# Optimization experiments

Hardware: AMD Instinct MI355X
Metric: run time of the kernel (lower is better)

Reference implementation:

```python
import jax, jax.numpy as jnp
import numpy as np

HIDDEN = 4096
N_HEADS = 32
N_KV = 8
HEAD_DIM = HIDDEN // N_HEADS  # 128
EPS = 1e-6
THETA = 10000.0
T = 2048


def _rms_norm(x, w, eps=EPS):
    # x: [T, H, D]; normalize over last dim
    var = jnp.mean(jnp.square(x), axis=-1, keepdims=True)
    return x * jax.lax.rsqrt(var + eps) * w


def _rope(pos, q, k, theta=THETA):
    # pos: [T] int; q: [T, Hq, D]; k: [T, Hk, D]  (rotate-half / NeoX style)
    d = q.shape[-1]
    inv_freq = 1.0 / (theta ** (jnp.arange(0, d, 2, dtype=jnp.float32) / d))  # [D/2]
    ang = pos.astype(jnp.float32)[:, None] * inv_freq  # [T, D/2]
    cos = jnp.cos(ang)[:, None, :]  # [T, 1, D/2]
    sin = jnp.sin(ang)[:, None, :]

    def rot(x):
        x1, x2 = jnp.split(x, 2, axis=-1)
        return jnp.concatenate([x1 * cos - x2 * sin, x2 * cos + x1 * sin], axis=-1)

    return rot(q), rot(k)


def setup_inputs() -> dict:
    key = jax.random.key(0)
    ks = jax.random.split(key, 4)
    x = jax.random.normal(ks[0], (T, HIDDEN), dtype=jnp.float32)
    pos = jnp.arange(T, dtype=jnp.int32)
    qkv_w = jax.random.normal(ks[1], (HIDDEN, HEAD_DIM * (N_HEADS + 2 * N_KV)), dtype=jnp.float32) * (HIDDEN ** -0.5)
    q_norm_w = jnp.ones((HEAD_DIM,), dtype=jnp.float32)
    k_norm_w = jnp.ones((HEAD_DIM,), dtype=jnp.float32)
    o_w = jax.random.normal(ks[2], (HIDDEN, HIDDEN), dtype=jnp.float32) * (HIDDEN ** -0.5)
    return {"x": x, "pos": pos, "qkv_w": qkv_w, "q_norm_w": q_norm_w,
            "k_norm_w": k_norm_w, "o_w": o_w}


def reference(x, pos, qkv_w, q_norm_w, k_norm_w, o_w):
    q_size = N_HEADS * HEAD_DIM
    kv_size = N_KV * HEAD_DIM
    qkv = x @ qkv_w  # [T, q+2kv]
    q, k, v = jnp.split(qkv, [q_size, q_size + kv_size], axis=-1)
    q = q.reshape(T, N_HEADS, HEAD_DIM)
    k = k.reshape(T, N_KV, HEAD_DIM)
    v = v.reshape(T, N_KV, HEAD_DIM)
    # per-head RMSNorm on q/k (qkv_bias=False path)
    q = _rms_norm(q, q_norm_w)
    k = _rms_norm(k, k_norm_w)
    q, k = _rope(pos, q, k)
    # GQA: expand kv heads to query heads
    g = N_HEADS // N_KV
    k = jnp.repeat(k, g, axis=1)  # [T, Hq, D]
    v = jnp.repeat(v, g, axis=1)
    scale = HEAD_DIM ** -0.5
    scores = jnp.einsum('thd,shd->hts', q, k) * scale  # [H, T, T]
    causal = jnp.tril(jnp.ones((T, T), dtype=bool))
    scores = jnp.where(causal[None], scores, jnp.finfo(scores.dtype).min)
    p = jax.nn.softmax(scores, axis=-1)
    o = jnp.einsum('hts,shd->thd', p, v).reshape(T, HIDDEN)
    return o @ o_w
```

## Files before the change

kernel.cpp:

```cpp
#include <hip/hip_runtime.h>
#include <hip/hip_bf16.h>

using u16 = unsigned short;
typedef __bf16 bf16x8 __attribute__((ext_vector_type(8)));
typedef float f32x4 __attribute__((ext_vector_type(4)));
typedef u16 u16x8 __attribute__((ext_vector_type(8)));
typedef u16 u16x4 __attribute__((ext_vector_type(4)));

constexpr int T_SEQ = 2048;
constexpr int HID   = 4096;
constexpr int NH    = 32;
constexpr int NKV   = 8;
constexpr int HD    = 128;
constexpr int QKVN  = 6144;

__device__ __forceinline__ u16 f2b(float x) {
  return __builtin_bit_cast(u16, __float2bfloat16(x));
}
__device__ __forceinline__ float b2f(u16 u) {
  return __builtin_bit_cast(float, (unsigned int)u << 16);
}
__device__ __forceinline__ bf16x8 load8(const u16* p) {
  return __builtin_bit_cast(bf16x8, *reinterpret_cast<const u16x8*>(p));
}
__device__ __forceinline__ f32x4 mfma16(bf16x8 a, bf16x8 b, f32x4 c) {
  return __builtin_amdgcn_mfma_f32_16x16x32_bf16(a, b, c, 0, 0, 0);
}

__global__ __launch_bounds__(256) void k_cast_bf16(const float* __restrict__ in,
                                                   u16* __restrict__ out, int n4) {
  int i = blockIdx.x * 256 + threadIdx.x;
  if (i < n4) {
    float4 v = reinterpret_cast<const float4*>(in)[i];
    u16x4 o;
    o.x = f2b(v.x); o.y = f2b(v.y); o.z = f2b(v.z); o.w = f2b(v.w);
    reinterpret_cast<u16x4*>(out)[i] = o;
  }
}

__global__ __launch_bounds__(256) void k_transpose_cast(const float* __restrict__ in,
                                                        u16* __restrict__ out,
                                                        int R, int C) {
  __shared__ float tile[32][33];
  int cc = blockIdx.x << 5, rr = blockIdx.y << 5;
  int lx = threadIdx.x & 31, ly = threadIdx.x >> 5;
#pragma unroll
  for (int i = 0; i < 32; i += 8)
    tile[ly + i][lx] = in[(size_t)(rr + ly + i) * C + cc + lx];
  __syncthreads();
#pragma unroll
  for (int i = 0; i < 32; i += 8)
    out[(size_t)(cc + ly + i) * R + rr + lx] = f2b(tile[lx][ly + i]);
}

template <int N, int K, typename OutT>
__global__ __launch_bounds__(256) void k_gemm_bt(const u16* __restrict__ A,
                                                 const u16* __restrict__ B,
                                                 OutT* __restrict__ C) {
  __shared__ u16 lA[128 * 32];
  __shared__ u16 lB[128 * 32];
  const int tid = threadIdx.x;
  const int wid = tid >> 6, lane = tid & 63;
  const int row0 = blockIdx.y << 7, col0 = blockIdx.x << 7;
  const int wr = wid >> 1, wc = wid & 1;
  const int g = lane >> 4, c = lane & 15;

  f32x4 acc[4][4] = {};

  const int r_st = lane >> 2;
  const int slot_st = lane & 3;

  const int rA0 = wr * 64 + c;
  const int rB0 = wc * 64 + c;
  const int swzA = (rA0 >> 1) & 3;
  const int swzB = (rB0 >> 1) & 3;

  for (int kt = 0; kt < K / 32; ++kt) {
    const int kk = kt * 32;
#pragma unroll
    for (int i = 0; i < 2; ++i) {
      int r = wid * 16 + i * 64 + r_st;
      int s = slot_st ^ ((r >> 1) & 3);
      const u16* ga = A + (size_t)(row0 + r) * K + kk + s * 8;
      const u16* gb = B + (size_t)(col0 + r) * K + kk + s * 8;
      char* la = (char*)lA + wid * 1024 + i * 4096;
      char* lb = (char*)lB + wid * 1024 + i * 4096;
      __builtin_amdgcn_global_load_lds((const __attribute__((address_space(1))) void*)ga,
                                       (__attribute__((address_space(3))) void*)la, 16, 0, 0);
      __builtin_amdgcn_global_load_lds((const __attribute__((address_space(1))) void*)gb,
                                       (__attribute__((address_space(3))) void*)lb, 16, 0, 0);
    }
    __syncthreads();

    bf16x8 af[4], bfr[4];
#pragma unroll
    for (int m = 0; m < 4; ++m) {
      int row = rA0 + m * 16;
      af[m] = load8(lA + row * 32 + (g ^ swzA) * 8);
    }
#pragma unroll
    for (int n = 0; n < 4; ++n) {
      int row = rB0 + n * 16;
      bfr[n] = load8(lB + row * 32 + (g ^ swzB) * 8);
    }
#pragma unroll
    for (int m = 0; m < 4; ++m)
#pragma unroll
      for (int n = 0; n < 4; ++n)
        acc[m][n] = mfma16(af[m], bfr[n], acc[m][n]);
    __syncthreads();
  }

#pragma unroll
  for (int m = 0; m < 4; ++m) {
    int grow0 = row0 + wr * 64 + m * 16 + g * 4;
#pragma unroll
    for (int n = 0; n < 4; ++n) {
      int gcol = col0 + wc * 64 + n * 16 + c;
#pragma unroll
      for (int j = 0; j < 4; ++j) {
        float v = acc[m][n][j];
        if constexpr (sizeof(OutT) == 2)
          C[(size_t)(grow0 + j) * N + gcol] = f2b(v);
        else
          C[(size_t)(grow0 + j) * N + gcol] = v;
      }
    }
  }
}

__global__ __launch_bounds__(256) void k_normrope(const u16* __restrict__ qkv,
                                                  const int* __restrict__ pos,
                                                  const float* __restrict__ qw,
                                                  const float* __restrict__ kw,
                                                  u16* __restrict__ qo,
                                                  u16* __restrict__ ko,
                                                  u16* __restrict__ vo) {
  int t = blockIdx.x;
  int wid = threadIdx.x >> 6, lane = threadIdx.x & 63;
  int h = blockIdx.y * 4 + wid;
  const u16* src = qkv + (size_t)t * QKVN + h * HD;
  float x1 = b2f(src[lane]), x2 = b2f(src[lane + 64]);
  float ss = x1 * x1 + x2 * x2;
#pragma unroll
  for (int m = 1; m < 64; m <<= 1) ss += __shfl_xor(ss, m);
  float sc = rsqrtf(ss * (1.0f / HD) + 1e-6f);
  if (h < 40) {
    const float* w = (h < NH) ? qw : kw;
    float y1 = x1 * sc * w[lane], y2 = x2 * sc * w[lane + 64];
    float p = (float)pos[t];
    float inv = exp2f((float)lane * (-13.287712379549449f / 64.0f));
    float ang = p * inv;
    float sn, cs;
    sincosf(ang, &sn, &cs);
    float o1 = y1 * cs - y2 * sn;
    float o2 = y2 * cs + y1 * sn;
    if (h < NH) {
      o1 *= 0.08838834764831845f;
      o2 *= 0.08838834764831845f;
      u16* dst = qo + ((size_t)t * NH + h) * HD;
      dst[lane] = f2b(o1);
      dst[lane + 64] = f2b(o2);
    } else {
      u16* dst = ko + ((size_t)t * NKV + (h - NH)) * HD;
      dst[lane] = f2b(o1);
      dst[lane + 64] = f2b(o2);
    }
  } else {
    u16* dst = vo + ((size_t)t * NKV + (h - 40)) * HD;
    dst[lane] = f2b(x1);
    dst[lane + 64] = f2b(x2);
  }
}

__global__ __launch_bounds__(256) void k_transpose_v(const u16* __restrict__ vb,
                                                     u16* __restrict__ vt) {
  __shared__ u16 tile[32][33];
  int tt = blockIdx.x << 5, dd = blockIdx.y << 5, h = blockIdx.z;
  int lx = threadIdx.x & 31, ly = threadIdx.x >> 5;
#pragma unroll
  for (int i = 0; i < 32; i += 8)
    tile[ly + i][lx] = vb[((size_t)(tt + ly + i) * NKV + h) * HD + dd + lx];
  __syncthreads();
#pragma unroll
  for (int i = 0; i < 32; i += 8)
    vt[((size_t)h * HD + dd + ly + i) * T_SEQ + tt + lx] = tile[lx][ly + i];
}

__global__ __launch_bounds__(256) void k_attn(const u16* __restrict__ qb,
                                              const u16* __restrict__ kbg,
                                              const u16* __restrict__ vtg,
                                              u16* __restrict__ out) {
  __shared__ u16 sK[2][64 * 128];
  __shared__ u16 sV[2][128 * 64];
  const int wid = threadIdx.x >> 6, lane = threadIdx.x & 63;
  const int h = blockIdx.y, hk = h >> 2;
  const int qt = gridDim.x - 1 - blockIdx.x;
  const int ntiles = qt + 1;
  const int qb0 = qt * 64 + wid * 16;
  const int g = lane >> 4, c = lane & 15;

  auto stage = [&](int buf, int kvb) {
#pragma unroll
    for (int ii = 0; ii < 4; ++ii) {
      int i = wid * 4 + ii;
      {
        int r = i * 4 + (lane >> 4);
        int slot = lane & 15;
        const u16* src = kbg + ((size_t)(kvb + r) * NKV + hk) * HD + ((slot ^ (r & 15)) * 8);
        __builtin_amdgcn_global_load_lds((const __attribute__((address_space(1))) void*)src,
                                         (__attribute__((address_space(3))) void*)((char*)sK[buf] + i * 1024),
                                         16, 0, 0);
      }
      {
        int d = i * 8 + (lane >> 3);
        int slot3 = lane & 7;
        const u16* src = vtg + ((size_t)hk * HD + d) * T_SEQ + kvb + ((slot3 ^ (d & 7)) * 8);
        __builtin_amdgcn_global_load_lds((const __attribute__((address_space(1))) void*)src,
                                         (__attribute__((address_space(3))) void*)((char*)sV[buf] + i * 1024),
                                         16, 0, 0);
      }
    }
  };

  bf16x8 qf[4];
  const u16* qrow = qb + ((size_t)(qb0 + c) * NH + h) * HD;
#pragma unroll
  for (int kc = 0; kc < 4; ++kc) qf[kc] = load8(qrow + kc * 32 + g * 8);

  f32x4 accO[8] = {};
  float m_ = -1e30f, l_ = 0.f;
  const int tq = qb0 + c;

  const int gh = g >> 1, gl4 = 4 * (g & 1), cx = c & 7;
  const int e0 = ((0 + gh) ^ cx) * 8 + gl4;
  const int e1 = ((2 + gh) ^ cx) * 8 + gl4;
  const int e2 = ((4 + gh) ^ cx) * 8 + gl4;
  const int e3 = ((6 + gh) ^ cx) * 8 + gl4;

  stage(0, 0);
  __syncthreads();

  for (int kt = 0; kt < ntiles; ++kt) {
    const int kvb = kt * 64;
    const int cur = kt & 1;
    if (kt + 1 < ntiles) stage(cur ^ 1, kvb + 64);

    f32x4 s[4];
#pragma unroll
    for (int tt = 0; tt < 4; ++tt) {
      const u16* kr = sK[cur] + (tt * 16 + c) * 128;
      f32x4 st = {0.f, 0.f, 0.f, 0.f};
#pragma unroll
      for (int kc = 0; kc < 4; ++kc) {
        int slot = (kc * 4 + g) ^ c;
        st = mfma16(load8(kr + slot * 8), qf[kc], st);
      }
      s[tt] = st;
    }

    float vmax = -1e30f;
#pragma unroll
    for (int tt = 0; tt < 4; ++tt)
#pragma unroll
      for (int j = 0; j < 4; ++j) {
        int tk = kvb + tt * 16 + 4 * g + j;
        float v = (tk <= tq) ? s[tt][j] : -1e30f;
        s[tt][j] = v;
        vmax = fmaxf(vmax, v);
      }
    vmax = fmaxf(vmax, __shfl_xor(vmax, 16));
    vmax = fmaxf(vmax, __shfl_xor(vmax, 32));
    float mn = fmaxf(m_, vmax);
    float a = __expf(m_ - mn);
    float ps = 0.f;
#pragma unroll
    for (int tt = 0; tt < 4; ++tt)
#pragma unroll
      for (int j = 0; j < 4; ++j) {
        float p = __expf(s[tt][j] - mn);
        s[tt][j] = p;
        ps += p;
      }
    ps += __shfl_xor(ps, 16);
    ps += __shfl_xor(ps, 32);
    l_ = l_ * a + ps;
    m_ = mn;

    float aq[4];
#pragma unroll
    for (int j = 0; j < 4; ++j) aq[j] = __shfl(a, 20 * g + j);
#pragma unroll
    for (int c2 = 0; c2 < 8; ++c2)
#pragma unroll
      for (int j = 0; j < 4; ++j) accO[c2][j] *= aq[j];

    u16x8 p0u, p1u;
#pragma unroll
    for (int j = 0; j < 4; ++j) {
      p0u[j]     = f2b(s[0][j]);
      p0u[j + 4] = f2b(s[1][j]);
      p1u[j]     = f2b(s[2][j]);
      p1u[j + 4] = f2b(s[3][j]);
    }
    bf16x8 p0 = __builtin_bit_cast(bf16x8, p0u);
    bf16x8 p1 = __builtin_bit_cast(bf16x8, p1u);

#pragma unroll
    for (int c2 = 0; c2 < 8; ++c2) {
      const u16* vr = sV[cur] + (c2 * 16 + c) * 64;
      u16x4 va  = *reinterpret_cast<const u16x4*>(vr + e0);
      u16x4 vb4 = *reinterpret_cast<const u16x4*>(vr + e1);
      u16x4 vc4 = *reinterpret_cast<const u16x4*>(vr + e2);
      u16x4 vd  = *reinterpret_cast<const u16x4*>(vr + e3);
      u16x8 v0u, v1u;
#pragma unroll
      for (int j = 0; j < 4; ++j) {
        v0u[j] = va[j];  v0u[j + 4] = vb4[j];
        v1u[j] = vc4[j]; v1u[j + 4] = vd[j];
      }
      accO[c2] = mfma16(p0, __builtin_bit_cast(bf16x8, v0u), accO[c2]);
      accO[c2] = mfma16(p1, __builtin_bit_cast(bf16x8, v1u), accO[c2]);
    }

    __syncthreads();
  }

  float lq[4];
#pragma unroll
  for (int j = 0; j < 4; ++j) lq[j] = 1.0f / __shfl(l_, 20 * g + j);
#pragma unroll
  for (int c2 = 0; c2 < 8; ++c2)
#pragma unroll
    for (int j = 0; j < 4; ++j) {
      float o = accO[c2][j] * lq[j];
      out[(size_t)(qb0 + 4 * g + j) * HID + h * HD + c2 * 16 + c] = f2b(o);
    }
}

extern "C" void kernel_launch(void* const* d_in, const int* in_sizes, int n_in,
                              void* d_out, int out_size, void* d_ws, size_t ws_size,
                              hipStream_t stream) {
  (void)in_sizes; (void)n_in; (void)out_size; (void)ws_size;
  const float* x      = (const float*)d_in[0];
  const int*   pos    = (const int*)d_in[1];
  const float* qkv_w  = (const float*)d_in[2];
  const float* qnw    = (const float*)d_in[3];
  const float* knw    = (const float*)d_in[4];
  const float* ow     = (const float*)d_in[5];
  float* out = (float*)d_out;
  char* ws = (char*)d_ws;

  u16* xb   = (u16*)(ws + 0);
  u16* attn = (u16*)(ws + 0);
  char* B0 = ws + 16777216;
  u16* qkv_wt = (u16*)B0;
  u16* qbuf = (u16*)(B0 + 0);
  u16* kbuf = (u16*)(B0 + 16777216);
  u16* vbuf = (u16*)(B0 + 20971520);
  u16* vtb  = (u16*)(B0 + 25165824);
  char* C0 = ws + 67108864;
  u16* qkvb = (u16*)C0;
  u16* o_wt = (u16*)C0;

  k_cast_bf16<<<dim3((T_SEQ * HID / 4 + 255) / 256), 256, 0, stream>>>(x, xb, T_SEQ * HID / 4);
  k_transpose_cast<<<dim3(QKVN / 32, HID / 32), 256, 0, stream>>>(qkv_w, qkv_wt, HID, QKVN);
  k_gemm_bt<QKVN, HID, u16><<<dim3(QKVN / 128, T_SEQ / 128), 256, 0, stream>>>(xb, qkv_wt, qkvb);
  k_normrope<<<dim3(T_SEQ, 12), 256, 0, stream>>>(qkvb, pos, qnw, knw, qbuf, kbuf, vbuf);
  k_transpose_v<<<dim3(T_SEQ / 32, HD / 32, NKV), 256, 0, stream>>>(vbuf, vtb);
  k_transpose_cast<<<dim3(HID / 32, HID / 32), 256, 0, stream>>>(ow, o_wt, HID, HID);
  k_attn<<<dim3(T_SEQ / 64, NH), 256, 0, stream>>>(qbuf, kbuf, vtb, attn);
  k_gemm_bt<HID, HID, float><<<dim3(HID / 128, T_SEQ / 128), 256, 0, stream>>>(attn, o_wt, out);
}
```

Measured before the change: 610.3 us.

## Replace GEMM with 256x256-tile 8-wave double-buffered pipelined kernel

```diff
diff --git a/kernel.cpp b/kernel.cpp
--- a/kernel.cpp
+++ b/kernel.cpp
@@ -26,6 +26,11 @@
 __device__ __forceinline__ f32x4 mfma16(bf16x8 a, bf16x8 b, f32x4 c) {
   return __builtin_amdgcn_mfma_f32_16x16x32_bf16(a, b, c, 0, 0, 0);
 }
+__device__ __forceinline__ void gload_lds16(const u16* src, u16* dst) {
+  __builtin_amdgcn_global_load_lds((const __attribute__((address_space(1))) void*)src,
+                                   (__attribute__((address_space(3))) void*)dst, 16, 0, 0);
+}
+#define BAR() asm volatile("s_barrier" ::: "memory")
 
 __global__ __launch_bounds__(256) void k_cast_bf16(const float* __restrict__ in,
                                                    u16* __restrict__ out, int n4) {
@@ -54,69 +59,110 @@
 }
 
 template <int N, int K, typename OutT>
-__global__ __launch_bounds__(256) void k_gemm_bt(const u16* __restrict__ A,
-                                                 const u16* __restrict__ B,
-                                                 OutT* __restrict__ C) {
-  __shared__ u16 lA[128 * 32];
-  __shared__ u16 lB[128 * 32];
+__global__ __launch_bounds__(512, 2) void k_gemm8(const u16* __restrict__ A,
+                                                  const u16* __restrict__ B,
+                                                  OutT* __restrict__ C) {
+  __shared__ u16 sA[2][256 * 64];
+  __shared__ u16 sB[2][256 * 64];
   const int tid = threadIdx.x;
   const int wid = tid >> 6, lane = tid & 63;
-  const int row0 = blockIdx.y << 7, col0 = blockIdx.x << 7;
-  const int wr = wid >> 1, wc = wid & 1;
   const int g = lane >> 4, c = lane & 15;
-
-  f32x4 acc[4][4] = {};
-
-  const int r_st = lane >> 2;
-  const int slot_st = lane & 3;
-
-  const int rA0 = wr * 64 + c;
-  const int rB0 = wc * 64 + c;
-  const int swzA = (rA0 >> 1) & 3;
-  const int swzB = (rB0 >> 1) & 3;
-
-  for (int kt = 0; kt < K / 32; ++kt) {
-    const int kk = kt * 32;
+  const int wm = wid >> 2, wn = wid & 3;
+
+  const int NWG = (T_SEQ / 256) * (N / 256);
+  const int wg = (blockIdx.x & 7) * (NWG / 8) + (blockIdx.x >> 3);
+  const int NBc = N / 256;
+  const int row0 = (wg / NBc) * 256, col0 = (wg % NBc) * 256;
+  const int NT = K / 64;
+
+  auto stage_half = [&](int h) {
+    const int T = h >> 2, k = h & 3;
+    const int buf = T & 1;
+    const int kk = T * 64;
+    const u16* gbase = (k < 2) ? A : B;
+    const int grow0 = ((k < 2) ? row0 : col0) + (k & 1) * 128;
+    u16* lbase = ((k < 2) ? sA[buf] : sB[buf]) + (k & 1) * (128 * 64);
 #pragma unroll
     for (int i = 0; i < 2; ++i) {
-      int r = wid * 16 + i * 64 + r_st;
-      int s = slot_st ^ ((r >> 1) & 3);
-      const u16* ga = A + (size_t)(row0 + r) * K + kk + s * 8;
-      const u16* gb = B + (size_t)(col0 + r) * K + kk + s * 8;
-      char* la = (char*)lA + wid * 1024 + i * 4096;
-      char* lb = (char*)lB + wid * 1024 + i * 4096;
-      __builtin_amdgcn_global_load_lds((const __attribute__((address_space(1))) void*)ga,
-                                       (__attribute__((address_space(3))) void*)la, 16, 0, 0);
-      __builtin_amdgcn_global_load_lds((const __attribute__((address_space(1))) void*)gb,
-                                       (__attribute__((address_space(3))) void*)lb, 16, 0, 0);
-    }
-    __syncthreads();
-
-    bf16x8 af[4], bfr[4];
+      int L = i * 512 + tid;
+      int r = L >> 3, seg = L & 7;
+      const u16* src = gbase + (size_t)(grow0 + r) * K + kk + ((seg ^ (r & 7)) * 8);
+      u16* dst = lbase + (i * 512 + wid * 64) * 8;
+      gload_lds16(src, dst);
+    }
+  };
+
+  f32x4 acc[8][4] = {};
+  bf16x8 a[4][2], b[4][2];
+
+  auto read_a = [&](int buf, int mbase) {
 #pragma unroll
     for (int m = 0; m < 4; ++m) {
-      int row = rA0 + m * 16;
-      af[m] = load8(lA + row * 32 + (g ^ swzA) * 8);
-    }
+      int r = wm * 128 + (mbase + m) * 16 + c;
+#pragma unroll
+      for (int k2 = 0; k2 < 2; ++k2) {
+        int q = k2 * 4 + g;
+        a[m][k2] = load8(sA[buf] + r * 64 + ((q ^ (r & 7)) * 8));
+      }
+    }
+  };
+  auto read_b = [&](int buf, int nbase) {
+#pragma unroll
+    for (int n = 0; n < 2; ++n) {
+      int r = wn * 64 + (nbase + n) * 16 + c;
+#pragma unroll
+      for (int k2 = 0; k2 < 2; ++k2) {
+        int q = k2 * 4 + g;
+        b[nbase + n][k2] = load8(sB[buf] + r * 64 + ((q ^ (r & 7)) * 8));
+      }
+    }
+  };
+  auto quad = [&](int mb, int nb) {
+    __builtin_amdgcn_s_setprio(1);
+#pragma unroll
+    for (int m = 0; m < 4; ++m)
+#pragma unroll
+      for (int n = 0; n < 2; ++n)
+#pragma unroll
+        for (int k2 = 0; k2 < 2; ++k2)
+          acc[mb + m][nb + n] = mfma16(a[m][k2], b[nb + n][k2], acc[mb + m][nb + n]);
+    __builtin_amdgcn_s_setprio(0);
+  };
+
+  stage_half(0); stage_half(1); stage_half(2); stage_half(3); stage_half(4);
+  asm volatile("s_waitcnt vmcnt(2)" ::: "memory");
+  BAR();
+
+  for (int kt = 0; kt < NT; ++kt) {
+    const int buf = kt & 1;
+    read_a(buf, 0); read_b(buf, 0);
+    if (4 * kt + 5 < 4 * NT) stage_half(4 * kt + 5);
+    BAR();
+    quad(0, 0);
+    BAR();
+    read_b(buf, 2);
+    if (4 * kt + 6 < 4 * NT) stage_half(4 * kt + 6);
+    BAR();
+    quad(0, 2);
+    BAR();
+    read_a(buf, 4);
+    if (4 * kt + 7 < 4 * NT) stage_half(4 * kt + 7);
+    BAR();
+    quad(4, 0);
+    BAR();
+    if (4 * kt + 8 < 4 * NT) stage_half(4 * kt + 8);
+    asm volatile("s_waitcnt vmcnt(2)" ::: "memory");
+    BAR();
+    quad(4, 2);
+    BAR();
+  }
+
+#pragma unroll
+  for (int m = 0; m < 8; ++m) {
+    int grow0 = row0 + wm * 128 + m * 16 + g * 4;
 #pragma unroll
     for (int n = 0; n < 4; ++n) {
-      int row = rB0 + n * 16;
-      bfr[n] = load8(lB + row * 32 + (g ^ swzB) * 8);
-    }
-#pragma unroll
-    for (int m = 0; m < 4; ++m)
-#pragma unroll
-      for (int n = 0; n < 4; ++n)
-        acc[m][n] = mfma16(af[m], bfr[n], acc[m][n]);
-    __syncthreads();
-  }
-
-#pragma unroll
-  for (int m = 0; m < 4; ++m) {
-    int grow0 = row0 + wr * 64 + m * 16 + g * 4;
-#pragma unroll
-    for (int n = 0; n < 4; ++n) {
-      int gcol = col0 + wc * 64 + n * 16 + c;
+      int gcol = col0 + wn * 64 + n * 16 + c;
 #pragma unroll
       for (int j = 0; j < 4; ++j) {
         float v = acc[m][n][j];
@@ -208,17 +254,13 @@
         int r = i * 4 + (lane >> 4);
         int slot = lane & 15;
         const u16* src = kbg + ((size_t)(kvb + r) * NKV + hk) * HD + ((slot ^ (r & 15)) * 8);
-        __builtin_amdgcn_global_load_lds((const __attribute__((address_space(1))) void*)src,
-                                         (__attribute__((address_space(3))) void*)((char*)sK[buf] + i * 1024),
-                                         16, 0, 0);
+        gload_lds16(src, (u16*)((char*)sK[buf] + i * 1024));
       }
       {
         int d = i * 8 + (lane >> 3);
         int slot3 = lane & 7;
         const u16* src = vtg + ((size_t)hk * HD + d) * T_SEQ + kvb + ((slot3 ^ (d & 7)) * 8);
-        __builtin_amdgcn_global_load_lds((const __attribute__((address_space(1))) void*)src,
-                                         (__attribute__((address_space(3))) void*)((char*)sV[buf] + i * 1024),
-                                         16, 0, 0);
+        gload_lds16(src, (u16*)((char*)sV[buf] + i * 1024));
       }
     }
   };
@@ -365,10 +407,10 @@
 
   k_cast_bf16<<<dim3((T_SEQ * HID / 4 + 255) / 256), 256, 0, stream>>>(x, xb, T_SEQ * HID / 4);
   k_transpose_cast<<<dim3(QKVN / 32, HID / 32), 256, 0, stream>>>(qkv_w, qkv_wt, HID, QKVN);
-  k_gemm_bt<QKVN, HID, u16><<<dim3(QKVN / 128, T_SEQ / 128), 256, 0, stream>>>(xb, qkv_wt, qkvb);
+  k_gemm8<QKVN, HID, u16><<<dim3((T_SEQ / 256) * (QKVN / 256)), 512, 0, stream>>>(xb, qkv_wt, qkvb);
   k_normrope<<<dim3(T_SEQ, 12), 256, 0, stream>>>(qkvb, pos, qnw, knw, qbuf, kbuf, vbuf);
   k_transpose_v<<<dim3(T_SEQ / 32, HD / 32, NKV), 256, 0, stream>>>(vbuf, vtb);
   k_transpose_cast<<<dim3(HID / 32, HID / 32), 256, 0, stream>>>(ow, o_wt, HID, HID);
   k_attn<<<dim3(T_SEQ / 64, NH), 256, 0, stream>>>(qbuf, kbuf, vtb, attn);
-  k_gemm_bt<HID, HID, float><<<dim3(HID / 128, T_SEQ / 128), 256, 0, stream>>>(attn, o_wt, out);
-}
+  k_gemm8<HID, HID, float><<<dim3((T_SEQ / 256) * (HID / 256)), 512, 0, stream>>>(attn, o_wt, out);
+}
```

Measured after the change: 650.5 us. 1.07x slower.
